# Optimization experiments

Measured on AMD Instinct MI355X. Metric: run time of the kernel, lower is better.

Reference implementation:

```python
import jax, jax.numpy as jnp
import numpy as np

C = 1024          # columns
K = 16            # cells per column
S = 32            # distal segments per cell
Y = 128           # synapses per segment
N = C * K         # num cells
PERM_THR = 0.5
ACT_THR = 10
LR = 0.1          # volatile learning rate
MOD = 1.0         # modulation_signal


def setup_inputs() -> dict:
    key = jax.random.key(0)
    k1, k2, k3, k4, k5 = jax.random.split(key, 5)
    x = jax.random.uniform(k1, (C,)) < 0.03                      # sparse column SDR
    prev_active_cells = jax.random.uniform(k2, (N,)) < 0.12      # prev-step active cells
    distal_connections = jax.random.randint(k3, (N, S, Y), 0, N, dtype=jnp.int32)
    volatile_permanences = jax.random.uniform(k4, (N, S, Y), dtype=jnp.float32)
    consolidated_permanences = jax.random.uniform(k5, (N, S, Y), dtype=jnp.float32) * 0.6
    return {
        "x": x,
        "prev_active_cells": prev_active_cells,
        "distal_connections": distal_connections,
        "volatile_permanences": volatile_permanences,
        "consolidated_permanences": consolidated_permanences,
    }


def reference(x, prev_active_cells, distal_connections, volatile_permanences, consolidated_permanences):
    conn = jnp.clip(distal_connections, 0, N - 1)                # [N,S,Y]
    x_active = x.astype(bool)                                    # [C]
    prev_any = prev_active_cells.any()

    # ---- phase 1: predictive state per column from prev_active_cells ----
    presyn_prev = prev_active_cells[conn]                        # [N,S,Y] irregular gather
    connected = (volatile_permanences > PERM_THR) | (consolidated_permanences > PERM_THR)
    active_syn = (connected & presyn_prev).sum(-1)               # [N,S]
    pred_cell = (active_syn >= ACT_THR).any(-1)                  # [N]
    pred_col = pred_cell.reshape(C, K)                           # [C,K]
    col_predicted = pred_col.any(-1)                             # [C]

    # ---- burst winner selection (unthresholded overlaps, argmax over K*S) ----
    overlaps = presyn_prev.sum(-1).astype(jnp.int32)             # [N,S]
    best_flat = jnp.argmax(overlaps.reshape(C, K * S), axis=-1)  # [C]
    burst_winner_local = best_flat // S                          # [C] (== 0 when no prev activity, matching torch fallback)
    burst_winner_mask = jax.nn.one_hot(burst_winner_local, K, dtype=bool)  # [C,K]

    winner = jnp.where(col_predicted[:, None], pred_col, burst_winner_mask)  # [C,K]
    winner = winner & x_active[:, None]                          # only active columns

    # new active cells: only bursting columns set cells (predicted columns set none, per source)
    new_active = jnp.broadcast_to((x_active & ~col_predicted)[:, None], (C, K))
    new_active_flat = new_active.reshape(-1)                     # [N]

    # ---- learning: update volatile permanences on each winner cell's best segment ----
    best_seg = jnp.argmax(overlaps, axis=-1)                     # [N]
    rows = jnp.arange(N)
    presyn_best = presyn_prev[rows, best_seg]                    # [N,Y]
    old_row = volatile_permanences[rows, best_seg]               # [N,Y]
    pot = LR * MOD
    pun = pot * 0.1
    new_row = jnp.clip(old_row + jnp.where(presyn_best, pot, -pun), 0.0, 1.0)
    learn_mask = winner.reshape(-1) & prev_any                   # [N] (torch skips learning if no prev activity)
    vol_new = volatile_permanences.at[rows, best_seg].set(
        jnp.where(learn_mask[:, None], new_row, old_row))

    # ---- phase 2: predictive state for next step from new active cells + updated perms ----
    presyn_new = new_active_flat[conn]                           # [N,S,Y]
    connected2 = (vol_new > PERM_THR) | (consolidated_permanences > PERM_THR)
    pred_next = (((connected2 & presyn_new).sum(-1)) >= ACT_THR).any(-1)  # [N]

    num_active = x_active.sum()
    num_pred = (x_active & col_predicted).sum()
    acc = jnp.where(num_active > 0,
                    num_pred.astype(jnp.float32) / jnp.maximum(num_active, 1).astype(jnp.float32),
                    jnp.float32(1.0))
    return new_active_flat, pred_next, acc
```

## Files before the change

### kernel.cpp

```cpp
#include <hip/hip_runtime.h>
#include <stdint.h>

#define C_ 1024
#define K_ 16
#define S_ 32
#define Y_ 128
#define N_ (C_ * K_)
#define ACT_THR 10
#define PERM_THR 0.5f
#define POT 0.1f
#define PUN 0.01f

#define WS_NUM_ACTIVE 0
#define WS_NUM_PRED   1
#define WS_NBURST     2
#define WS_LEARN_CNT  3
#define WS_PREV_ANY   4
#define WS_BURSTMASK  8
#define WS_PREVMASK   64
#define WS_CELLINFO   1024
#define WS_LIST       (1024 + N_)

#define P1_BLOCKS 2048

__global__ __launch_bounds__(512) void pack_kernel(const int* __restrict__ prev,
                                                   unsigned* __restrict__ ws) {
    const int tid = threadIdx.x;
    if (tid < 64) ws[tid] = 0u;
    __syncthreads();
    const int4* p = reinterpret_cast<const int4*>(prev + tid * 32);
    unsigned m = 0u;
    #pragma unroll
    for (int q = 0; q < 8; ++q) {
        const int4 v = p[q];
        m |= (v.x != 0 ? 1u : 0u) << (q * 4 + 0);
        m |= (v.y != 0 ? 1u : 0u) << (q * 4 + 1);
        m |= (v.z != 0 ? 1u : 0u) << (q * 4 + 2);
        m |= (v.w != 0 ? 1u : 0u) << (q * 4 + 3);
    }
    ws[WS_PREVMASK + tid] = m;
    const bool any = (__ballot(m != 0u) != 0ull);
    if ((tid & 63) == 0 && any) atomicOr(&ws[WS_PREV_ANY], 1u);
}

__global__ __launch_bounds__(256) void phase1_kernel(const int*   __restrict__ conn,
                                                     const float* __restrict__ vol,
                                                     const float* __restrict__ cons,
                                                     unsigned*    __restrict__ ws) {
    __shared__ unsigned prevmask[512];
    const int tid = threadIdx.x;
    for (int i = tid; i < 512; i += 256) prevmask[i] = ws[WS_PREVMASK + i];
    __syncthreads();

    const int wave = tid >> 6;
    const int lane = tid & 63;
    const int half = lane >> 5;
    const int l32  = lane & 31;
    const int sh   = half * 32;

    #pragma unroll 1
    for (int ci = 0; ci < 2; ++ci) {
        const int cell = blockIdx.x * 8 + wave + ci * 4;
        const size_t cellbase = (size_t)cell * (S_ * Y_) + (size_t)(l32 * 4);

        size_t a = cellbase + (size_t)half * Y_;
        int4   cv_n = *reinterpret_cast<const int4*>(conn + a);
        float4 vv_n = *reinterpret_cast<const float4*>(vol + a);
        float4 sv_n = *reinterpret_cast<const float4*>(cons + a);

        unsigned key = 0u;
        bool predf = false;

        #pragma unroll 2
        for (int i = 0; i < 16; ++i) {
            const int4   cv = cv_n;
            const float4 vv = vv_n;
            const float4 sv = sv_n;
            if (i < 15) {
                const size_t nb = cellbase + (size_t)(2 * (i + 1) + half) * Y_;
                cv_n = *reinterpret_cast<const int4*>(conn + nb);
                vv_n = *reinterpret_cast<const float4*>(vol + nb);
                sv_n = *reinterpret_cast<const float4*>(cons + nb);
            }

            const int m0 = min(max(cv.x, 0), N_ - 1);
            const int m1 = min(max(cv.y, 0), N_ - 1);
            const int m2 = min(max(cv.z, 0), N_ - 1);
            const int m3 = min(max(cv.w, 0), N_ - 1);
            const bool p0 = (prevmask[m0 >> 5] >> (m0 & 31)) & 1u;
            const bool p1 = (prevmask[m1 >> 5] >> (m1 & 31)) & 1u;
            const bool p2 = (prevmask[m2 >> 5] >> (m2 & 31)) & 1u;
            const bool p3 = (prevmask[m3 >> 5] >> (m3 & 31)) & 1u;
            const bool c0 = (vv.x > PERM_THR) || (sv.x > PERM_THR);
            const bool c1 = (vv.y > PERM_THR) || (sv.y > PERM_THR);
            const bool c2 = (vv.z > PERM_THR) || (sv.z > PERM_THR);
            const bool c3 = (vv.w > PERM_THR) || (sv.w > PERM_THR);

            const uint64_t bp0 = __ballot(p0), bp1 = __ballot(p1),
                           bp2 = __ballot(p2), bp3 = __ballot(p3);
            const uint64_t ba0 = __ballot(p0 && c0), ba1 = __ballot(p1 && c1),
                           ba2 = __ballot(p2 && c2), ba3 = __ballot(p3 && c3);

            const int ov = __popc((unsigned)(bp0 >> sh)) + __popc((unsigned)(bp1 >> sh)) +
                           __popc((unsigned)(bp2 >> sh)) + __popc((unsigned)(bp3 >> sh));
            const int ac = __popc((unsigned)(ba0 >> sh)) + __popc((unsigned)(ba1 >> sh)) +
                           __popc((unsigned)(ba2 >> sh)) + __popc((unsigned)(ba3 >> sh));

            predf |= (ac >= ACT_THR);
            const int seg = 2 * i + half;
            const unsigned k2 = ((unsigned)ov << 6) | (unsigned)(63 - seg);
            key = max(key, k2);
        }

        const unsigned okey = (unsigned)__shfl_xor((int)key, 32);
        const unsigned fkey = max(key, okey);
        const bool fpred = (__any(predf ? 1 : 0) != 0);
        if (lane == 0) {
            const int bo = (int)(fkey >> 6);
            const int bs = 63 - (int)(fkey & 63u);
            ws[WS_CELLINFO + cell] = (fpred ? 1u : 0u) | ((unsigned)bs << 8) | ((unsigned)bo << 16);
        }
    }
}

__global__ __launch_bounds__(256) void column_kernel(const int* __restrict__ x,
                                                     unsigned*  __restrict__ ws,
                                                     float*     __restrict__ out_new_active) {
    const int c = blockIdx.x * 256 + threadIdx.x;
    if (c >= C_) return;
    const bool xa = (x[c] != 0);
    const int base = c * K_;

    unsigned info[K_];
    bool colpred = false;
    int bo = -1, bk = 0;
    #pragma unroll
    for (int k = 0; k < K_; ++k) {
        const unsigned inf = ws[WS_CELLINFO + base + k];
        info[k] = inf;
        if (inf & 1u) colpred = true;
        const int ov = (int)((inf >> 16) & 0xFFu);
        if (ov > bo) { bo = ov; bk = k; }
    }

    const bool burst = xa && !colpred;
    const float nav = burst ? 1.0f : 0.0f;
    #pragma unroll
    for (int k = 0; k < K_; ++k) out_new_active[base + k] = nav;

    if (xa) {
        atomicAdd(&ws[WS_NUM_ACTIVE], 1u);
        if (colpred) atomicAdd(&ws[WS_NUM_PRED], 1u);
    }
    if (burst) {
        atomicAdd(&ws[WS_NBURST], 1u);
        atomicOr(&ws[WS_BURSTMASK + (c >> 5)], 1u << (c & 31));
    }
    if (xa) {
        if (colpred) {
            #pragma unroll
            for (int k = 0; k < K_; ++k) {
                if (info[k] & 1u) {
                    const unsigned i = atomicAdd(&ws[WS_LEARN_CNT], 1u);
                    ws[WS_LIST + i] = (unsigned)(base + k);
                }
            }
        } else {
            const unsigned i = atomicAdd(&ws[WS_LEARN_CNT], 1u);
            ws[WS_LIST + i] = (unsigned)(base + bk);
        }
    }
}

__global__ __launch_bounds__(256) void learn_kernel(const int* __restrict__ conn,
                                                    float*     __restrict__ vol,
                                                    unsigned*  __restrict__ ws,
                                                    float*     __restrict__ out_acc) {
    __shared__ unsigned prevmask[512];
    const int tid = threadIdx.x;
    for (int i = tid; i < 512; i += 256) prevmask[i] = ws[WS_PREVMASK + i];
    __syncthreads();

    if (blockIdx.x == 0 && tid == 0) {
        const int na  = (int)ws[WS_NUM_ACTIVE];
        const int np_ = (int)ws[WS_NUM_PRED];
        out_acc[0] = (na > 0) ? ((float)np_ / (float)na) : 1.0f;
    }
    if (ws[WS_PREV_ANY] == 0u) return;

    const int cnt    = (int)ws[WS_LEARN_CNT];
    const int wave   = (blockIdx.x * 256 + tid) >> 6;
    const int lane   = tid & 63;
    const int nwaves = gridDim.x * 4;

    for (int e = wave; e < cnt; e += nwaves) {
        const int cell = (int)ws[WS_LIST + e];
        const int seg  = (int)((ws[WS_CELLINFO + cell] >> 8) & 0xFFu);
        const size_t base = ((size_t)cell * S_ + seg) * Y_ + (size_t)(lane * 2);
        const int2 cv = *reinterpret_cast<const int2*>(conn + base);
        float2 vv = *reinterpret_cast<const float2*>(vol + base);
        const int m0 = min(max(cv.x, 0), N_ - 1);
        const int m1 = min(max(cv.y, 0), N_ - 1);
        const bool p0 = (prevmask[m0 >> 5] >> (m0 & 31)) & 1u;
        const bool p1 = (prevmask[m1 >> 5] >> (m1 & 31)) & 1u;
        vv.x = fminf(fmaxf(vv.x + (p0 ? POT : -PUN), 0.0f), 1.0f);
        vv.y = fminf(fmaxf(vv.y + (p1 ? POT : -PUN), 0.0f), 1.0f);
        *reinterpret_cast<float2*>(vol + base) = vv;
    }
}

__global__ __launch_bounds__(256) void phase2_kernel(const int*   __restrict__ conn,
                                                     const float* __restrict__ vol,
                                                     const float* __restrict__ cons,
                                                     const unsigned* __restrict__ ws,
                                                     float* __restrict__ out_pred_next) {
    __shared__ unsigned nburst_s;
    __shared__ unsigned burstmask[32];
    const int tid = threadIdx.x;
    if (tid == 0) nburst_s = ws[WS_NBURST];
    if (tid >= 64 && tid < 96) burstmask[tid - 64] = ws[WS_BURSTMASK + (tid - 64)];
    __syncthreads();

    const int cbase = blockIdx.x * 8;
    if (nburst_s == 0u) {
        if (tid < 8) out_pred_next[cbase + tid] = 0.0f;
        return;
    }

    const int wave = tid >> 6;
    const int lane = tid & 63;
    const int half = lane >> 5;
    const int l32  = lane & 31;
    const int sh   = half * 32;

    #pragma unroll 1
    for (int ci = 0; ci < 2; ++ci) {
        const int cell = cbase + wave + ci * 4;
        const size_t cellbase = (size_t)cell * (S_ * Y_) + (size_t)(l32 * 4);

        size_t a = cellbase + (size_t)half * Y_;
        int4   cv_n = *reinterpret_cast<const int4*>(conn + a);
        float4 vv_n = *reinterpret_cast<const float4*>(vol + a);
        float4 sv_n = *reinterpret_cast<const float4*>(cons + a);

        bool predf = false;

        #pragma unroll 2
        for (int i = 0; i < 16; ++i) {
            const int4   cv = cv_n;
            const float4 vv = vv_n;
            const float4 sv = sv_n;
            if (i < 15) {
                const size_t nb = cellbase + (size_t)(2 * (i + 1) + half) * Y_;
                cv_n = *reinterpret_cast<const int4*>(conn + nb);
                vv_n = *reinterpret_cast<const float4*>(vol + nb);
                sv_n = *reinterpret_cast<const float4*>(cons + nb);
            }

            const int m0 = min(max(cv.x, 0), N_ - 1) >> 4;
            const int m1 = min(max(cv.y, 0), N_ - 1) >> 4;
            const int m2 = min(max(cv.z, 0), N_ - 1) >> 4;
            const int m3 = min(max(cv.w, 0), N_ - 1) >> 4;
            const bool p0 = (burstmask[m0 >> 5] >> (m0 & 31)) & 1u;
            const bool p1 = (burstmask[m1 >> 5] >> (m1 & 31)) & 1u;
            const bool p2 = (burstmask[m2 >> 5] >> (m2 & 31)) & 1u;
            const bool p3 = (burstmask[m3 >> 5] >> (m3 & 31)) & 1u;
            const bool c0 = (vv.x > PERM_THR) || (sv.x > PERM_THR);
            const bool c1 = (vv.y > PERM_THR) || (sv.y > PERM_THR);
            const bool c2 = (vv.z > PERM_THR) || (sv.z > PERM_THR);
            const bool c3 = (vv.w > PERM_THR) || (sv.w > PERM_THR);

            const uint64_t ba0 = __ballot(p0 && c0), ba1 = __ballot(p1 && c1),
                           ba2 = __ballot(p2 && c2), ba3 = __ballot(p3 && c3);
            const int ac = __popc((unsigned)(ba0 >> sh)) + __popc((unsigned)(ba1 >> sh)) +
                           __popc((unsigned)(ba2 >> sh)) + __popc((unsigned)(ba3 >> sh));
            predf |= (ac >= ACT_THR);
        }

        const bool fpred = (__any(predf ? 1 : 0) != 0);
        if (lane == 0) out_pred_next[cell] = fpred ? 1.0f : 0.0f;
    }
}

extern "C" void kernel_launch(void* const* d_in, const int* in_sizes, int n_in,
                              void* d_out, int out_size, void* d_ws, size_t ws_size,
                              hipStream_t stream) {
    const int*   x    = (const int*)d_in[0];
    const int*   prev = (const int*)d_in[1];
    const int*   conn = (const int*)d_in[2];
    float*       vol  = (float*)d_in[3];
    const float* cons = (const float*)d_in[4];
    float*    out = (float*)d_out;
    unsigned* ws  = (unsigned*)d_ws;

    pack_kernel  <<<1,        512, 0, stream>>>(prev, ws);
    phase1_kernel<<<P1_BLOCKS, 256, 0, stream>>>(conn, vol, cons, ws);
    column_kernel<<<C_ / 256,  256, 0, stream>>>(x, ws, out);
    learn_kernel <<<64,        256, 0, stream>>>(conn, vol, ws, out + 2 * N_);
    phase2_kernel<<<P1_BLOCKS, 256, 0, stream>>>(conn, vol, cons, ws, out + N_);
}
```

Baseline: 673.0 us.

## Precompute packed connected-synapse bitmask once and reuse across both prediction phases

Adds a precompute pass that reduces the volatile and consolidated permanence tensors into a packed per-synapse connected bitmask in workspace. Both prediction phases then read only the connection indices plus this small bitmask, instead of re-reading both float permanence tensors. The learn step patches the bitmask nibbles for the updated segments so phase 2 sees the new permanences. This cuts repeated large float reads at the cost of an extra kernel pass and a dependency on workspace size, with the original path kept as a fallback.

```diff
diff --git a/kernel.cpp b/kernel.cpp
--- a/kernel.cpp
+++ b/kernel.cpp
@@ -20,8 +20,8 @@
 #define WS_PREVMASK   64
 #define WS_CELLINFO   1024
 #define WS_LIST       (1024 + N_)
-
-#define P1_BLOCKS 2048
+#define WS_CONBITS    65536
+
 
 __global__ __launch_bounds__(512) void pack_kernel(const int* __restrict__ prev,
                                                    unsigned* __restrict__ ws) {
@@ -43,10 +43,44 @@
     if ((tid & 63) == 0 && any) atomicOr(&ws[WS_PREV_ANY], 1u);
 }
 
-__global__ __launch_bounds__(256) void phase1_kernel(const int*   __restrict__ conn,
-                                                     const float* __restrict__ vol,
-                                                     const float* __restrict__ cons,
-                                                     unsigned*    __restrict__ ws) {
+__global__ __launch_bounds__(256) void precompute_kernel(const float* __restrict__ vol,
+                                                         const float* __restrict__ cons,
+                                                         unsigned long long* __restrict__ conbits) {
+    const int tid  = threadIdx.x;
+    const int wave = tid >> 6;
+    const int lane = tid & 63;
+    const int half = lane >> 5;
+    const int l32  = lane & 31;
+    const int cell = blockIdx.x * 4 + wave;
+    const size_t base = (size_t)cell * (S_ * Y_) + (size_t)half * Y_ + (size_t)(l32 * 4);
+
+    float4 v0 = *reinterpret_cast<const float4*>(vol  + base);
+    float4 s0 = *reinterpret_cast<const float4*>(cons + base);
+    float4 v1 = *reinterpret_cast<const float4*>(vol  + base + 256);
+    float4 s1 = *reinterpret_cast<const float4*>(cons + base + 256);
+
+    unsigned long long bits = 0ull;
+    #pragma unroll 4
+    for (int i = 0; i < 16; ++i) {
+        const float4 vv = v0, sv = s0;
+        v0 = v1; s0 = s1;
+        if (i < 14) {
+            const size_t nb = base + (size_t)(i + 2) * 256;
+            v1 = *reinterpret_cast<const float4*>(vol  + nb);
+            s1 = *reinterpret_cast<const float4*>(cons + nb);
+        }
+        const unsigned nib = ((vv.x > PERM_THR || sv.x > PERM_THR) ? 1u : 0u)
+                           | ((vv.y > PERM_THR || sv.y > PERM_THR) ? 2u : 0u)
+                           | ((vv.z > PERM_THR || sv.z > PERM_THR) ? 4u : 0u)
+                           | ((vv.w > PERM_THR || sv.w > PERM_THR) ? 8u : 0u);
+        bits |= ((unsigned long long)nib) << (4 * i);
+    }
+    conbits[(size_t)cell * 64 + lane] = bits;
+}
+
+__global__ __launch_bounds__(256) void phase1b_kernel(const int* __restrict__ conn,
+                                                      const unsigned long long* __restrict__ conbits,
+                                                      unsigned* __restrict__ ws) {
     __shared__ unsigned prevmask[512];
     const int tid = threadIdx.x;
     for (int i = tid; i < 512; i += 256) prevmask[i] = ws[WS_PREVMASK + i];
@@ -57,69 +91,61 @@
     const int half = lane >> 5;
     const int l32  = lane & 31;
     const int sh   = half * 32;
-
-    #pragma unroll 1
-    for (int ci = 0; ci < 2; ++ci) {
-        const int cell = blockIdx.x * 8 + wave + ci * 4;
-        const size_t cellbase = (size_t)cell * (S_ * Y_) + (size_t)(l32 * 4);
-
-        size_t a = cellbase + (size_t)half * Y_;
-        int4   cv_n = *reinterpret_cast<const int4*>(conn + a);
-        float4 vv_n = *reinterpret_cast<const float4*>(vol + a);
-        float4 sv_n = *reinterpret_cast<const float4*>(cons + a);
-
-        unsigned key = 0u;
-        bool predf = false;
-
-        #pragma unroll 2
-        for (int i = 0; i < 16; ++i) {
-            const int4   cv = cv_n;
-            const float4 vv = vv_n;
-            const float4 sv = sv_n;
-            if (i < 15) {
-                const size_t nb = cellbase + (size_t)(2 * (i + 1) + half) * Y_;
-                cv_n = *reinterpret_cast<const int4*>(conn + nb);
-                vv_n = *reinterpret_cast<const float4*>(vol + nb);
-                sv_n = *reinterpret_cast<const float4*>(cons + nb);
-            }
-
-            const int m0 = min(max(cv.x, 0), N_ - 1);
-            const int m1 = min(max(cv.y, 0), N_ - 1);
-            const int m2 = min(max(cv.z, 0), N_ - 1);
-            const int m3 = min(max(cv.w, 0), N_ - 1);
-            const bool p0 = (prevmask[m0 >> 5] >> (m0 & 31)) & 1u;
-            const bool p1 = (prevmask[m1 >> 5] >> (m1 & 31)) & 1u;
-            const bool p2 = (prevmask[m2 >> 5] >> (m2 & 31)) & 1u;
-            const bool p3 = (prevmask[m3 >> 5] >> (m3 & 31)) & 1u;
-            const bool c0 = (vv.x > PERM_THR) || (sv.x > PERM_THR);
-            const bool c1 = (vv.y > PERM_THR) || (sv.y > PERM_THR);
-            const bool c2 = (vv.z > PERM_THR) || (sv.z > PERM_THR);
-            const bool c3 = (vv.w > PERM_THR) || (sv.w > PERM_THR);
-
-            const uint64_t bp0 = __ballot(p0), bp1 = __ballot(p1),
-                           bp2 = __ballot(p2), bp3 = __ballot(p3);
-            const uint64_t ba0 = __ballot(p0 && c0), ba1 = __ballot(p1 && c1),
-                           ba2 = __ballot(p2 && c2), ba3 = __ballot(p3 && c3);
-
-            const int ov = __popc((unsigned)(bp0 >> sh)) + __popc((unsigned)(bp1 >> sh)) +
-                           __popc((unsigned)(bp2 >> sh)) + __popc((unsigned)(bp3 >> sh));
-            const int ac = __popc((unsigned)(ba0 >> sh)) + __popc((unsigned)(ba1 >> sh)) +
-                           __popc((unsigned)(ba2 >> sh)) + __popc((unsigned)(ba3 >> sh));
-
-            predf |= (ac >= ACT_THR);
-            const int seg = 2 * i + half;
-            const unsigned k2 = ((unsigned)ov << 6) | (unsigned)(63 - seg);
-            key = max(key, k2);
-        }
-
-        const unsigned okey = (unsigned)__shfl_xor((int)key, 32);
-        const unsigned fkey = max(key, okey);
-        const bool fpred = (__any(predf ? 1 : 0) != 0);
-        if (lane == 0) {
-            const int bo = (int)(fkey >> 6);
-            const int bs = 63 - (int)(fkey & 63u);
-            ws[WS_CELLINFO + cell] = (fpred ? 1u : 0u) | ((unsigned)bs << 8) | ((unsigned)bo << 16);
-        }
+    const int cell = blockIdx.x * 4 + wave;
+    const size_t base = (size_t)cell * (S_ * Y_) + (size_t)half * Y_ + (size_t)(l32 * 4);
+
+    unsigned long long bits = conbits[(size_t)cell * 64 + lane];
+    int4 a0 = *reinterpret_cast<const int4*>(conn + base);
+    int4 a1 = *reinterpret_cast<const int4*>(conn + base + 256);
+
+    unsigned key = 0u;
+    bool predf = false;
+
+    #pragma unroll 4
+    for (int i = 0; i < 16; ++i) {
+        const int4 cv = a0;
+        a0 = a1;
+        if (i < 14) a1 = *reinterpret_cast<const int4*>(conn + base + (size_t)(i + 2) * 256);
+
+        const unsigned nib = (unsigned)bits & 0xFu;
+        bits >>= 4;
+
+        const int m0 = min(max(cv.x, 0), N_ - 1);
+        const int m1 = min(max(cv.y, 0), N_ - 1);
+        const int m2 = min(max(cv.z, 0), N_ - 1);
+        const int m3 = min(max(cv.w, 0), N_ - 1);
+        const bool p0 = (prevmask[m0 >> 5] >> (m0 & 31)) & 1u;
+        const bool p1 = (prevmask[m1 >> 5] >> (m1 & 31)) & 1u;
+        const bool p2 = (prevmask[m2 >> 5] >> (m2 & 31)) & 1u;
+        const bool p3 = (prevmask[m3 >> 5] >> (m3 & 31)) & 1u;
+        const bool c0 = nib & 1u;
+        const bool c1 = nib & 2u;
+        const bool c2 = nib & 4u;
+        const bool c3 = nib & 8u;
+
+        const uint64_t bp0 = __ballot(p0), bp1 = __ballot(p1),
+                       bp2 = __ballot(p2), bp3 = __ballot(p3);
+        const uint64_t ba0 = __ballot(p0 && c0), ba1 = __ballot(p1 && c1),
+                       ba2 = __ballot(p2 && c2), ba3 = __ballot(p3 && c3);
+
+        const int ov = __popc((unsigned)(bp0 >> sh)) + __popc((unsigned)(bp1 >> sh)) +
+                       __popc((unsigned)(bp2 >> sh)) + __popc((unsigned)(bp3 >> sh));
+        const int ac = __popc((unsigned)(ba0 >> sh)) + __popc((unsigned)(ba1 >> sh)) +
+                       __popc((unsigned)(ba2 >> sh)) + __popc((unsigned)(ba3 >> sh));
+
+        predf |= (ac >= ACT_THR);
+        const int seg = 2 * i + half;
+        const unsigned k2 = ((unsigned)ov << 6) | (unsigned)(63 - seg);
+        key = max(key, k2);
+    }
+
+    const unsigned okey = (unsigned)__shfl_xor((int)key, 32);
+    const unsigned fkey = max(key, okey);
+    const bool fpred = (__any(predf ? 1 : 0) != 0);
+    if (lane == 0) {
+        const int bo = (int)(fkey >> 6);
+        const int bs = 63 - (int)(fkey & 63u);
+        ws[WS_CELLINFO + cell] = (fpred ? 1u : 0u) | ((unsigned)bs << 8) | ((unsigned)bo << 16);
     }
 }
 
@@ -172,10 +198,211 @@
     }
 }
 
-__global__ __launch_bounds__(256) void learn_kernel(const int* __restrict__ conn,
-                                                    float*     __restrict__ vol,
-                                                    unsigned*  __restrict__ ws,
-                                                    float*     __restrict__ out_acc) {
+__global__ __launch_bounds__(256) void learnb_kernel(const int*   __restrict__ conn,
+                                                     float*       __restrict__ vol,
+                                                     const float* __restrict__ cons,
+                                                     unsigned*    __restrict__ ws,
+                                                     float*       __restrict__ out_acc) {
+    __shared__ unsigned prevmask[512];
+    const int tid = threadIdx.x;
+    for (int i = tid; i < 512; i += 256) prevmask[i] = ws[WS_PREVMASK + i];
+    __syncthreads();
+
+    if (blockIdx.x == 0 && tid == 0) {
+        const int na  = (int)ws[WS_NUM_ACTIVE];
+        const int np_ = (int)ws[WS_NUM_PRED];
+        out_acc[0] = (na > 0) ? ((float)np_ / (float)na) : 1.0f;
+    }
+    if (ws[WS_PREV_ANY] == 0u) return;
+
+    const int cnt = (int)ws[WS_LEARN_CNT];
+    const int hw  = (blockIdx.x * 256 + tid) >> 5;
+    const int g   = tid & 31;
+    const int nhw = gridDim.x * 8;
+    unsigned* conbits32 = ws + WS_CONBITS;
+
+    for (int e = hw; e < cnt; e += nhw) {
+        const int cellv = (int)ws[WS_LIST + e];
+        const int seg   = (int)((ws[WS_CELLINFO + cellv] >> 8) & 0xFFu);
+        const size_t base = ((size_t)cellv * S_ + seg) * Y_ + (size_t)(g * 4);
+        const int4   cv = *reinterpret_cast<const int4*>(conn + base);
+        float4       vv = *reinterpret_cast<float4*>(vol + base);
+        const float4 sv = *reinterpret_cast<const float4*>(cons + base);
+        const int m0 = min(max(cv.x, 0), N_ - 1);
+        const int m1 = min(max(cv.y, 0), N_ - 1);
+        const int m2 = min(max(cv.z, 0), N_ - 1);
+        const int m3 = min(max(cv.w, 0), N_ - 1);
+        const bool p0 = (prevmask[m0 >> 5] >> (m0 & 31)) & 1u;
+        const bool p1 = (prevmask[m1 >> 5] >> (m1 & 31)) & 1u;
+        const bool p2 = (prevmask[m2 >> 5] >> (m2 & 31)) & 1u;
+        const bool p3 = (prevmask[m3 >> 5] >> (m3 & 31)) & 1u;
+        vv.x = fminf(fmaxf(vv.x + (p0 ? POT : -PUN), 0.0f), 1.0f);
+        vv.y = fminf(fmaxf(vv.y + (p1 ? POT : -PUN), 0.0f), 1.0f);
+        vv.z = fminf(fmaxf(vv.z + (p2 ? POT : -PUN), 0.0f), 1.0f);
+        vv.w = fminf(fmaxf(vv.w + (p3 ? POT : -PUN), 0.0f), 1.0f);
+        *reinterpret_cast<float4*>(vol + base) = vv;
+
+        const unsigned nib = ((vv.x > PERM_THR || sv.x > PERM_THR) ? 1u : 0u)
+                           | ((vv.y > PERM_THR || sv.y > PERM_THR) ? 2u : 0u)
+                           | ((vv.z > PERM_THR || sv.z > PERM_THR) ? 4u : 0u)
+                           | ((vv.w > PERM_THR || sv.w > PERM_THR) ? 8u : 0u);
+        const int chunk = seg >> 1;
+        const int slot  = (seg & 1) * 32 + g;
+        const unsigned idx = (unsigned)(cellv * 128 + slot * 2 + (chunk >> 3));
+        const int shn = 4 * (chunk & 7);
+        const unsigned old = conbits32[idx];
+        conbits32[idx] = (old & ~(0xFu << shn)) | (nib << shn);
+    }
+}
+
+__global__ __launch_bounds__(256) void phase2b_kernel(const int* __restrict__ conn,
+                                                      const unsigned long long* __restrict__ conbits,
+                                                      const unsigned* __restrict__ ws,
+                                                      float* __restrict__ out_pred_next) {
+    __shared__ unsigned nburst_s;
+    __shared__ unsigned burstmask[32];
+    const int tid = threadIdx.x;
+    if (tid == 0) nburst_s = ws[WS_NBURST];
+    if (tid >= 64 && tid < 96) burstmask[tid - 64] = ws[WS_BURSTMASK + (tid - 64)];
+    __syncthreads();
+
+    const int cbase = blockIdx.x * 4;
+    if (nburst_s == 0u) {
+        if (tid < 4) out_pred_next[cbase + tid] = 0.0f;
+        return;
+    }
+
+    const int wave = tid >> 6;
+    const int lane = tid & 63;
+    const int half = lane >> 5;
+    const int l32  = lane & 31;
+    const int sh   = half * 32;
+    const int cell = cbase + wave;
+    const size_t base = (size_t)cell * (S_ * Y_) + (size_t)half * Y_ + (size_t)(l32 * 4);
+
+    unsigned long long bits = conbits[(size_t)cell * 64 + lane];
+    int4 a0 = *reinterpret_cast<const int4*>(conn + base);
+    int4 a1 = *reinterpret_cast<const int4*>(conn + base + 256);
+
+    bool predf = false;
+
+    #pragma unroll 4
+    for (int i = 0; i < 16; ++i) {
+        const int4 cv = a0;
+        a0 = a1;
+        if (i < 14) a1 = *reinterpret_cast<const int4*>(conn + base + (size_t)(i + 2) * 256);
+
+        const unsigned nib = (unsigned)bits & 0xFu;
+        bits >>= 4;
+
+        const int m0 = min(max(cv.x, 0), N_ - 1) >> 4;
+        const int m1 = min(max(cv.y, 0), N_ - 1) >> 4;
+        const int m2 = min(max(cv.z, 0), N_ - 1) >> 4;
+        const int m3 = min(max(cv.w, 0), N_ - 1) >> 4;
+        const bool p0 = (burstmask[m0 >> 5] >> (m0 & 31)) & 1u;
+        const bool p1 = (burstmask[m1 >> 5] >> (m1 & 31)) & 1u;
+        const bool p2 = (burstmask[m2 >> 5] >> (m2 & 31)) & 1u;
+        const bool p3 = (burstmask[m3 >> 5] >> (m3 & 31)) & 1u;
+        const bool c0 = nib & 1u;
+        const bool c1 = nib & 2u;
+        const bool c2 = nib & 4u;
+        const bool c3 = nib & 8u;
+
+        const uint64_t ba0 = __ballot(p0 && c0), ba1 = __ballot(p1 && c1),
+                       ba2 = __ballot(p2 && c2), ba3 = __ballot(p3 && c3);
+        const int ac = __popc((unsigned)(ba0 >> sh)) + __popc((unsigned)(ba1 >> sh)) +
+                       __popc((unsigned)(ba2 >> sh)) + __popc((unsigned)(ba3 >> sh));
+        predf |= (ac >= ACT_THR);
+    }
+
+    const bool fpred = (__any(predf ? 1 : 0) != 0);
+    if (lane == 0) out_pred_next[cell] = fpred ? 1.0f : 0.0f;
+}
+
+__global__ __launch_bounds__(256) void phase1_old(const int*   __restrict__ conn,
+                                                  const float* __restrict__ vol,
+                                                  const float* __restrict__ cons,
+                                                  unsigned*    __restrict__ ws) {
+    __shared__ unsigned prevmask[512];
+    const int tid = threadIdx.x;
+    for (int i = tid; i < 512; i += 256) prevmask[i] = ws[WS_PREVMASK + i];
+    __syncthreads();
+
+    const int wave = tid >> 6;
+    const int lane = tid & 63;
+    const int half = lane >> 5;
+    const int l32  = lane & 31;
+    const int sh   = half * 32;
+
+    #pragma unroll 1
+    for (int ci = 0; ci < 2; ++ci) {
+        const int cell = blockIdx.x * 8 + wave + ci * 4;
+        const size_t cellbase = (size_t)cell * (S_ * Y_) + (size_t)(l32 * 4);
+
+        size_t a = cellbase + (size_t)half * Y_;
+        int4   cv_n = *reinterpret_cast<const int4*>(conn + a);
+        float4 vv_n = *reinterpret_cast<const float4*>(vol + a);
+        float4 sv_n = *reinterpret_cast<const float4*>(cons + a);
+
+        unsigned key = 0u;
+        bool predf = false;
+
+        #pragma unroll 2
+        for (int i = 0; i < 16; ++i) {
+            const int4   cv = cv_n;
+            const float4 vv = vv_n;
+            const float4 sv = sv_n;
+            if (i < 15) {
+                const size_t nb = cellbase + (size_t)(2 * (i + 1) + half) * Y_;
+                cv_n = *reinterpret_cast<const int4*>(conn + nb);
+                vv_n = *reinterpret_cast<const float4*>(vol + nb);
+                sv_n = *reinterpret_cast<const float4*>(cons + nb);
+            }
+
+            const int m0 = min(max(cv.x, 0), N_ - 1);
+            const int m1 = min(max(cv.y, 0), N_ - 1);
+            const int m2 = min(max(cv.z, 0), N_ - 1);
+            const int m3 = min(max(cv.w, 0), N_ - 1);
+            const bool p0 = (prevmask[m0 >> 5] >> (m0 & 31)) & 1u;
+            const bool p1 = (prevmask[m1 >> 5] >> (m1 & 31)) & 1u;
+            const bool p2 = (prevmask[m2 >> 5] >> (m2 & 31)) & 1u;
+            const bool p3 = (prevmask[m3 >> 5] >> (m3 & 31)) & 1u;
+            const bool c0 = (vv.x > PERM_THR) || (sv.x > PERM_THR);
+            const bool c1 = (vv.y > PERM_THR) || (sv.y > PERM_THR);
+            const bool c2 = (vv.z > PERM_THR) || (sv.z > PERM_THR);
+            const bool c3 = (vv.w > PERM_THR) || (sv.w > PERM_THR);
+
+            const uint64_t bp0 = __ballot(p0), bp1 = __ballot(p1),
+                           bp2 = __ballot(p2), bp3 = __ballot(p3);
+            const uint64_t ba0 = __ballot(p0 && c0), ba1 = __ballot(p1 && c1),
+                           ba2 = __ballot(p2 && c2), ba3 = __ballot(p3 && c3);
+
+            const int ov = __popc((unsigned)(bp0 >> sh)) + __popc((unsigned)(bp1 >> sh)) +
+                           __popc((unsigned)(bp2 >> sh)) + __popc((unsigned)(bp3 >> sh));
+            const int ac = __popc((unsigned)(ba0 >> sh)) + __popc((unsigned)(ba1 >> sh)) +
+                           __popc((unsigned)(ba2 >> sh)) + __popc((unsigned)(ba3 >> sh));
+
+            predf |= (ac >= ACT_THR);
+            const int seg = 2 * i + half;
+            const unsigned k2 = ((unsigned)ov << 6) | (unsigned)(63 - seg);
+            key = max(key, k2);
+        }
+
+        const unsigned okey = (unsigned)__shfl_xor((int)key, 32);
+        const unsigned fkey = max(key, okey);
+        const bool fpred = (__any(predf ? 1 : 0) != 0);
+        if (lane == 0) {
+            const int bo = (int)(fkey >> 6);
+            const int bs = 63 - (int)(fkey & 63u);
+            ws[WS_CELLINFO + cell] = (fpred ? 1u : 0u) | ((unsigned)bs << 8) | ((unsigned)bo << 16);
+        }
+    }
+}
+
+__global__ __launch_bounds__(256) void learn_old(const int* __restrict__ conn,
+                                                 float*     __restrict__ vol,
+                                                 unsigned*  __restrict__ ws,
+                                                 float*     __restrict__ out_acc) {
     __shared__ unsigned prevmask[512];
     const int tid = threadIdx.x;
     for (int i = tid; i < 512; i += 256) prevmask[i] = ws[WS_PREVMASK + i];
@@ -209,11 +436,11 @@
     }
 }
 
-__global__ __launch_bounds__(256) void phase2_kernel(const int*   __restrict__ conn,
-                                                     const float* __restrict__ vol,
-                                                     const float* __restrict__ cons,
-                                                     const unsigned* __restrict__ ws,
-                                                     float* __restrict__ out_pred_next) {
+__global__ __launch_bounds__(256) void phase2_old(const int*   __restrict__ conn,
+                                                  const float* __restrict__ vol,
+                                                  const float* __restrict__ cons,
+                                                  const unsigned* __restrict__ ws,
+                                                  float* __restrict__ out_pred_next) {
     __shared__ unsigned nburst_s;
     __shared__ unsigned burstmask[32];
     const int tid = threadIdx.x;
@@ -293,9 +520,21 @@
     float*    out = (float*)d_out;
     unsigned* ws  = (unsigned*)d_ws;
 
-    pack_kernel  <<<1,        512, 0, stream>>>(prev, ws);
-    phase1_kernel<<<P1_BLOCKS, 256, 0, stream>>>(conn, vol, cons, ws);
-    column_kernel<<<C_ / 256,  256, 0, stream>>>(x, ws, out);
-    learn_kernel <<<64,        256, 0, stream>>>(conn, vol, ws, out + 2 * N_);
-    phase2_kernel<<<P1_BLOCKS, 256, 0, stream>>>(conn, vol, cons, ws, out + N_);
-}
+    const size_t need = (size_t)WS_CONBITS * 4 + (size_t)N_ * 64 * 8;
+
+    pack_kernel<<<1, 512, 0, stream>>>(prev, ws);
+
+    if (ws_size >= need) {
+        unsigned long long* conbits = (unsigned long long*)(ws + WS_CONBITS);
+        precompute_kernel<<<N_ / 4, 256, 0, stream>>>(vol, cons, conbits);
+        phase1b_kernel   <<<N_ / 4, 256, 0, stream>>>(conn, conbits, ws);
+        column_kernel    <<<C_ / 256, 256, 0, stream>>>(x, ws, out);
+        learnb_kernel    <<<64, 256, 0, stream>>>(conn, vol, cons, ws, out + 2 * N_);
+        phase2b_kernel   <<<N_ / 4, 256, 0, stream>>>(conn, conbits, ws, out + N_);
+    } else {
+        phase1_old<<<2048, 256, 0, stream>>>(conn, vol, cons, ws);
+        column_kernel<<<C_ / 256, 256, 0, stream>>>(x, ws, out);
+        learn_old<<<64, 256, 0, stream>>>(conn, vol, ws, out + 2 * N_);
+        phase2_old<<<2048, 256, 0, stream>>>(conn, vol, cons, ws, out + N_);
+    }
+}
```

Measured after the change: 680.6 us. Within noise of the previous version (+1.1%).
